# Performance work log

Hardware: AMD Instinct MI355X
Metric: run time of the kernel (lower is better)

Reference implementation:

```python
import jax, jax.numpy as jnp
import numpy as np

EPS = 1e-4

@jax.custom_vjp
def bin_active(x):
    # BinActive: sign forward, straight-through (hard-tanh) backward
    return jnp.sign(x)

def _ba_fwd(x):
    return jnp.sign(x), x

def _ba_bwd(x, g):
    return (g * (jnp.abs(x) <= 1.0).astype(g.dtype),)

bin_active.defvjp(_ba_fwd, _ba_bwd)

def norm_bin(x):
    # per-node mean/std (torch .std is unbiased, ddof=1) then binarize
    x = x - jnp.mean(x, axis=1, keepdims=True)
    x = x / (jnp.std(x, axis=1, ddof=1, keepdims=True) + EPS)
    return bin_active(x)

def bin_weight(W):
    # XNOR-style weight binarization: per-output-row scale * sign(W)
    alpha = jnp.mean(jnp.abs(W), axis=1, keepdims=True)
    return alpha * jnp.sign(W)

def bi_sage_conv(x_src, x_tgt, edge_index, W_l, W_r, b):
    # mean-aggregate source messages onto targets, then two binarized linears
    src, dst = edge_index[0], edge_index[1]
    n_tgt = x_tgt.shape[0]
    msg = x_src[src]                                             # [E, F] gather
    agg = jax.ops.segment_sum(msg, dst, num_segments=n_tgt)       # [n_tgt, F]
    cnt = jax.ops.segment_sum(jnp.ones((src.shape[0],), x_src.dtype), dst,
                              num_segments=n_tgt)
    agg = agg / jnp.maximum(cnt, 1.0)[:, None]
    out = agg @ bin_weight(W_l).T + x_tgt @ bin_weight(W_r).T + b
    return out


def setup_inputs() -> dict:
    key = jax.random.key(0)
    ks = jax.random.split(key, 10)
    N0, N1, B = 292864, 11264, 1024
    F_IN, F_HID, F_OUT = 602, 256, 41
    E1, E2 = 281600, 10240
    x = jax.random.normal(ks[0], (N0, F_IN), dtype=jnp.float32)
    # bipartite edges: row0 = source idx in [0, n_src), row1 = target idx in [0, n_tgt)
    ei1 = jnp.stack([jax.random.randint(ks[1], (E1,), 0, N0),
                     jax.random.randint(ks[2], (E1,), 0, N1)]).astype(jnp.int64)
    ei2 = jnp.stack([jax.random.randint(ks[3], (E2,), 0, N1),
                     jax.random.randint(ks[4], (E2,), 0, B)]).astype(jnp.int64)
    s1 = 0.1
    return {
        "x": x,
        "edge_index1": ei1,
        "edge_index2": ei2,
        "n1": N1,
        "n_batch": B,
        "W1_l": s1 * jax.random.normal(ks[5], (F_HID, F_IN), dtype=jnp.float32),
        "W1_r": s1 * jax.random.normal(ks[6], (F_HID, F_IN), dtype=jnp.float32),
        "b1": jnp.zeros((F_HID,), jnp.float32),
        "W2_l": s1 * jax.random.normal(ks[7], (F_OUT, F_HID), dtype=jnp.float32),
        "W2_r": s1 * jax.random.normal(ks[8], (F_OUT, F_HID), dtype=jnp.float32),
        "b2": jnp.zeros((F_OUT,), jnp.float32),
    }


def reference(x, edge_index1, edge_index2, n1, n_batch,
              W1_l, W1_r, b1, W2_l, W2_r, b2):
    # layer 1
    x_t = x[:n1]
    h = bi_sage_conv(norm_bin(x), norm_bin(x_t), edge_index1, W1_l, W1_r, b1)
    h = jax.nn.relu(h)  # dropout p=0.0 -> identity
    # layer 2
    h_t = h[:n_batch]
    out = bi_sage_conv(norm_bin(h), norm_bin(h_t), edge_index2, W2_l, W2_r, b2)
    return jax.nn.log_softmax(out, axis=-1)
```

## Files before the change

kernel.cpp:

```cpp
#include <hip/hip_runtime.h>
#include <hip/hip_bf16.h>
#include <cstdint>
#include <cstddef>

#define CDIV(a,b) (((a)+(b)-1)/(b))

using bf16x8 = __attribute__((ext_vector_type(8))) short;
using f32x4  = __attribute__((ext_vector_type(4))) float;

struct __align__(8) F4 { float x, y, z, w; };
struct __align__(8) F2 { float x, y; };

__device__ __forceinline__ unsigned short sgn_bf16(float s){
  return (s > 0.f) ? 0x3F80u : ((s < 0.f) ? 0xBF80u : 0u);
}

__device__ __forceinline__ int colX(int k){
  int w = k >> 5, b = k & 31;
  if (w < 16){
    int g = w >> 3, wr = w & 7;
    int j = wr >> 1, half = wr & 1;
    return 256*g + 4*(32*half + b) + j;
  }
  int j = w - 16;
  int c = 512 + 4*b + j;
  return (c < 602) ? c : -1;
}
__device__ __forceinline__ int colH(int k){
  int w = k >> 5, b = k & 31;
  int j = w >> 1, half = w & 1;
  return 4*(32*half + b) + j;
}

__global__ void prep_all(const float* __restrict__ W1l, const float* __restrict__ W1r,
                         const float* __restrict__ W2l, const float* __restrict__ W2r,
                         float* __restrict__ aL, float* __restrict__ aR,
                         float* __restrict__ a2L, float* __restrict__ a2R,
                         int* __restrict__ degB, int ndeg,
                         unsigned short* __restrict__ bsgn,
                         unsigned char* __restrict__ mask, int n0, int n1){
  int r = blockIdx.x;
  if (r < 594){
    const float* wr; float* dst; int K;
    if (r < 256){ wr = W1l + (size_t)r*602; dst = aL + r; K = 602; }
    else if (r < 512){ int q = r-256; wr = W1r + (size_t)q*602; dst = aR + q; K = 602; }
    else if (r < 553){ int q = r-512; wr = W2l + (size_t)q*256; dst = a2L + q; K = 256; }
    else { int q = r-553; wr = W2r + (size_t)q*256; dst = a2R + q; K = 256; }
    float s = 0.f;
    for (int k = threadIdx.x; k < K; k += blockDim.x) s += fabsf(wr[k]);
    #pragma unroll
    for (int off = 32; off; off >>= 1) s += __shfl_xor(s, off);
    __shared__ float red[4];
    int wid = threadIdx.x >> 6, lane = threadIdx.x & 63;
    if (lane == 0) red[wid] = s;
    __syncthreads();
    if (threadIdx.x == 0) *dst = (red[0]+red[1]+red[2]+red[3]) / (float)K;
  } else if (r < 642){
    int i = (r - 594)*256 + threadIdx.x;
    if (i < ndeg) degB[i] = 0;
  } else if (r < 1922){
    int idx = (r - 642)*256 + threadIdx.x;
    if (idx < 256*1280){
      int o = idx / 1280, k = idx - o*1280;
      float v = 0.f;
      if (k < 640){ int c = colX(k);       if (c >= 0) v = W1l[(size_t)o*602 + c]; }
      else        { int c = colX(k - 640); if (c >= 0) v = W1r[(size_t)o*602 + c]; }
      bsgn[idx] = sgn_bf16(v);
    }
  } else {
    int i = (r - 1922)*256 + threadIdx.x;
    if (i < n0) mask[i] = (i < n1) ? 1 : 0;
  }
}

__global__ void mark_count(const int* __restrict__ s1, const int* __restrict__ d1, int E1,
                           unsigned char* __restrict__ mask, int* __restrict__ deg1,
                           const int* __restrict__ d2, int E2, int* __restrict__ deg2){
  int e = blockIdx.x*blockDim.x + threadIdx.x;
  if (e < E1){
    mask[s1[e]] = 1;
    atomicAdd(&deg1[d1[e]], 1);
  } else if (e < E1 + E2){
    atomicAdd(&deg2[d2[e - E1]], 1);
  }
}

__global__ void pack_scan_bcat(const float* __restrict__ X, uint32_t* __restrict__ P, int nrows,
                               const unsigned char* __restrict__ mask, int packBlocks,
                               const int* __restrict__ deg1, int* __restrict__ rs1, int* __restrict__ cur1, int n1c,
                               const int* __restrict__ deg2, int* __restrict__ rs2, int* __restrict__ cur2, int n2c,
                               const float* __restrict__ W2l, const float* __restrict__ W2r,
                               const float* __restrict__ a2L, const float* __restrict__ a2R,
                               float* __restrict__ Bcat2){
  __shared__ int partial[256];
  const int bid = blockIdx.x;
  if (bid >= packBlocks){
    int role = bid - packBlocks;
    if (role < 2){
      const int* deg = role ? deg2 : deg1;
      int* rs  = role ? rs2  : rs1;
      int* cur = role ? cur2 : cur1;
      int n    = role ? n2c  : n1c;
      int tid = threadIdx.x;
      int per = CDIV(n, 256);
      int begin = tid*per; if (begin > n) begin = n;
      int end = begin + per; if (end > n) end = n;
      int s = 0;
      for (int i = begin; i < end; ++i) s += deg[i];
      partial[tid] = s;
      __syncthreads();
      for (int off = 1; off < 256; off <<= 1){
        int add = (tid >= off) ? partial[tid-off] : 0;
        __syncthreads();
        partial[tid] += add;
        __syncthreads();
      }
      int prefix = (tid == 0) ? 0 : partial[tid-1];
      for (int i = begin; i < end; ++i){ rs[i] = prefix; cur[i] = prefix; prefix += deg[i]; }
      if (tid == 255) rs[n] = prefix;
    } else {
      int idx = (role - 2)*256 + threadIdx.x;
      if (idx < 512*41){
        int o = idx % 41, k = idx / 41;
        int c = (k < 256) ? colH(k) : colH(k - 256);
        float w = (k < 256) ? W2l[(size_t)o*256 + c] : W2r[(size_t)o*256 + c];
        float a = (k < 256) ? a2L[o] : a2R[o];
        float sg = (w > 0.f) ? 1.f : ((w < 0.f) ? -1.f : 0.f);
        Bcat2[idx] = a * sg;
      }
    }
    return;
  }
  const int row = bid*4 + (threadIdx.x >> 6);
  const int lane = threadIdx.x & 63;
  if (row >= nrows) return;
  if (!mask[row]) return;
  const float* xr = X + (size_t)row * 602;
  F4 v0 = *(const F4*)&xr[4*lane];
  F4 v1 = *(const F4*)&xr[256 + 4*lane];
  F4 v2 = {0.f,0.f,0.f,0.f};
  if (lane < 22) v2 = *(const F4*)&xr[512 + 4*lane];
  else if (lane == 22){ F2 t = *(const F2*)&xr[600]; v2.x = t.x; v2.y = t.y; }
  float s = v0.x+v0.y+v0.z+v0.w + v1.x+v1.y+v1.z+v1.w + v2.x+v2.y+v2.z+v2.w;
  #pragma unroll
  for (int off = 32; off; off >>= 1) s += __shfl_xor(s, off);
  const float mean = s / 602.f;
  uint32_t wpos[20], wneg[20];
  {
    float d0 = v0.x - mean, d1v = v0.y - mean, d2v = v0.z - mean, d3 = v0.w - mean;
    unsigned long long b0 = __ballot(d0 > 0.f), b1 = __ballot(d1v > 0.f),
                       b2 = __ballot(d2v > 0.f), b3 = __ballot(d3 > 0.f);
    wpos[0]=(uint32_t)b0; wpos[1]=(uint32_t)(b0>>32); wpos[2]=(uint32_t)b1; wpos[3]=(uint32_t)(b1>>32);
    wpos[4]=(uint32_t)b2; wpos[5]=(uint32_t)(b2>>32); wpos[6]=(uint32_t)b3; wpos[7]=(uint32_t)(b3>>32);
    b0 = __ballot(d0 < 0.f); b1 = __ballot(d1v < 0.f); b2 = __ballot(d2v < 0.f); b3 = __ballot(d3 < 0.f);
    wneg[0]=(uint32_t)b0; wneg[1]=(uint32_t)(b0>>32); wneg[2]=(uint32_t)b1; wneg[3]=(uint32_t)(b1>>32);
    wneg[4]=(uint32_t)b2; wneg[5]=(uint32_t)(b2>>32); wneg[6]=(uint32_t)b3; wneg[7]=(uint32_t)(b3>>32);
  }
  {
    float d0 = v1.x - mean, d1v = v1.y - mean, d2v = v1.z - mean, d3 = v1.w - mean;
    unsigned long long b0 = __ballot(d0 > 0.f), b1 = __ballot(d1v > 0.f),
                       b2 = __ballot(d2v > 0.f), b3 = __ballot(d3 > 0.f);
    wpos[8]=(uint32_t)b0; wpos[9]=(uint32_t)(b0>>32); wpos[10]=(uint32_t)b1; wpos[11]=(uint32_t)(b1>>32);
    wpos[12]=(uint32_t)b2; wpos[13]=(uint32_t)(b2>>32); wpos[14]=(uint32_t)b3; wpos[15]=(uint32_t)(b3>>32);
    b0 = __ballot(d0 < 0.f); b1 = __ballot(d1v < 0.f); b2 = __ballot(d2v < 0.f); b3 = __ballot(d3 < 0.f);
    wneg[8]=(uint32_t)b0; wneg[9]=(uint32_t)(b0>>32); wneg[10]=(uint32_t)b1; wneg[11]=(uint32_t)(b1>>32);
    wneg[12]=(uint32_t)b2; wneg[13]=(uint32_t)(b2>>32); wneg[14]=(uint32_t)b3; wneg[15]=(uint32_t)(b3>>32);
  }
  {
    int base = 4*lane;
    float d0 = v2.x - mean, d1v = v2.y - mean, d2v = v2.z - mean, d3 = v2.w - mean;
    wpos[16] = (uint32_t)__ballot((base+0 < 90) && (d0 > 0.f));
    wpos[17] = (uint32_t)__ballot((base+1 < 90) && (d1v > 0.f));
    wpos[18] = (uint32_t)__ballot((base+2 < 90) && (d2v > 0.f));
    wpos[19] = (uint32_t)__ballot((base+3 < 90) && (d3 > 0.f));
    wneg[16] = (uint32_t)__ballot((base+0 < 90) && (d0 < 0.f));
    wneg[17] = (uint32_t)__ballot((base+1 < 90) && (d1v < 0.f));
    wneg[18] = (uint32_t)__ballot((base+2 < 90) && (d2v < 0.f));
    wneg[19] = (uint32_t)__ballot((base+3 < 90) && (d3 < 0.f));
  }
  if (lane == 0){
    uint32_t* pr = P + (size_t)row * 40;
    #pragma unroll
    for (int q = 0; q < 5; ++q){
      uint4 a; a.x = wpos[4*q]; a.y = wpos[4*q+1]; a.z = wpos[4*q+2]; a.w = wpos[4*q+3];
      *(uint4*)&pr[4*q] = a;
      uint4 b; b.x = wneg[4*q]; b.y = wneg[4*q+1]; b.z = wneg[4*q+2]; b.w = wneg[4*q+3];
      *(uint4*)&pr[20 + 4*q] = b;
    }
  }
}

__global__ void fill_both(const int* __restrict__ s1, const int* __restrict__ d1, int E1,
                          int* __restrict__ cur1, int* __restrict__ esrc1,
                          const int* __restrict__ s2, const int* __restrict__ d2, int E2,
                          int* __restrict__ cur2, int* __restrict__ esrc2){
  int e = blockIdx.x*blockDim.x + threadIdx.x;
  if (e < E1){
    int p = atomicAdd(&cur1[d1[e]], 1);
    esrc1[p] = s1[e];
  } else if (e < E1 + E2){
    int q = e - E1;
    int p = atomicAdd(&cur2[d2[q]], 1);
    esrc2[p] = s2[q];
  }
}

__global__ void aggregate_v3(const uint32_t* __restrict__ packed,
                             const int* __restrict__ rs, const int* __restrict__ esrc,
                             unsigned short* __restrict__ S, float* __restrict__ invdeg){
  const int t = blockIdx.x;
  const int lane = threadIdx.x;
  const int slot = lane / 20;
  const int w = lane - slot*20;
  const int s0 = rs[t], s1 = rs[t+1];
  const bool active = slot < 3;
  uint32_t p[8] = {0,0,0,0,0,0,0,0};
  uint32_t n[8] = {0,0,0,0,0,0,0,0};
  for (int base = s0; base < s1; base += 3){
    int e = base + slot;
    uint32_t wp = 0, wn = 0;
    if (active && e < s1){
      const uint32_t* pr = packed + (size_t)esrc[e] * 40;
      wp = pr[w];
      wn = pr[20 + w];
    }
    #pragma unroll
    for (int b = 0; b < 8; ++b){
      p[b] += (wp >> b) & 0x01010101u;
      n[b] += (wn >> b) & 0x01010101u;
    }
  }
  #pragma unroll
  for (int b = 0; b < 8; ++b){
    p[b] += __shfl(p[b], lane + 20) + __shfl(p[b], lane + 40);
    n[b] += __shfl(n[b], lane + 20) + __shfl(n[b], lane + 40);
  }
  if (lane == 0){
    int deg = s1 - s0;
    invdeg[t] = 1.f / (float)(deg > 0 ? deg : 1);
  }
  if (lane < 20){
    unsigned short* sr = S + (size_t)t * 640;
    #pragma unroll
    for (int b = 0; b < 8; ++b){
      #pragma unroll
      for (int k = 0; k < 4; ++k){
        int col = 32*lane + b + 8*k;
        int cnt = (int)((p[b] >> (8*k)) & 0xFF) - (int)((n[b] >> (8*k)) & 0xFF);
        float f = (float)cnt;
        sr[col] = (unsigned short)(__float_as_uint(f) >> 16);
      }
    }
  }
}

__global__ __launch_bounds__(256) void gemm1_fused(
    const unsigned short* __restrict__ Sx, const uint32_t* __restrict__ packedX,
    const unsigned short* __restrict__ bsgn, const float* __restrict__ invdeg,
    const float* __restrict__ aL, const float* __restrict__ aR,
    const float* __restrict__ bias, uint32_t* __restrict__ packedH){
  __shared__ __align__(16) char smem[33792];
  unsigned short (*As)[40] = (unsigned short (*)[40])smem;
  unsigned short (*Bs)[40] = (unsigned short (*)[40])(smem + 32*40*2);
  float (*Hs)[264] = (float (*)[264])smem;

  const int tid = threadIdx.x;
  const int lane = tid & 63, wid = tid >> 6;
  const int m0 = blockIdx.x * 32;
  const int frow = lane & 15, fk = (lane >> 4) * 8;
  const int sRow = tid >> 3, sK = (tid & 7) * 4;

  f32x4 acc1[2][4], acc2[2][4];
  #pragma unroll
  for (int i = 0; i < 2; ++i)
    #pragma unroll
    for (int j = 0; j < 4; ++j){ f32x4 z = {0.f,0.f,0.f,0.f}; acc1[i][j] = z; acc2[i][j] = z; }

  const unsigned short* SxRow = Sx + (size_t)(m0 + sRow) * 640;
  const uint32_t* pxRow = packedX + (size_t)(m0 + sRow) * 40;
  const unsigned short* bsgnCol = bsgn + (size_t)tid * 1280;

  for (int kc = 0; kc < 640; kc += 32){
    *(uint2*)&As[sRow][sK] = *(const uint2*)&SxRow[kc + sK];
    *(bf16x8*)&Bs[tid][0]  = *(const bf16x8*)&bsgnCol[kc];
    *(bf16x8*)&Bs[tid][8]  = *(const bf16x8*)&bsgnCol[kc + 8];
    *(bf16x8*)&Bs[tid][16] = *(const bf16x8*)&bsgnCol[kc + 16];
    *(bf16x8*)&Bs[tid][24] = *(const bf16x8*)&bsgnCol[kc + 24];
    __syncthreads();
    bf16x8 a0 = *(bf16x8*)&As[frow][fk];
    bf16x8 a1 = *(bf16x8*)&As[16 + frow][fk];
    #pragma unroll
    for (int nf = 0; nf < 4; ++nf){
      bf16x8 b = *(bf16x8*)&Bs[wid*64 + nf*16 + frow][fk];
      acc1[0][nf] = __builtin_amdgcn_mfma_f32_16x16x32_bf16(a0, b, acc1[0][nf], 0, 0, 0);
      acc1[1][nf] = __builtin_amdgcn_mfma_f32_16x16x32_bf16(a1, b, acc1[1][nf], 0, 0, 0);
    }
    __syncthreads();
  }
  for (int kc = 0; kc < 640; kc += 32){
    int w = kc >> 5;
    {
      uint32_t wp = pxRow[w];
      uint32_t wq = pxRow[20 + w];
      union { unsigned short u[4]; uint2 v; } tmp;
      #pragma unroll
      for (int j = 0; j < 4; ++j){
        int b_ = sK + j;
        tmp.u[j] = ((wp >> b_) & 1) ? 0x3F80u : (((wq >> b_) & 1) ? 0xBF80u : 0u);
      }
      *(uint2*)&As[sRow][sK] = tmp.v;
    }
    *(bf16x8*)&Bs[tid][0]  = *(const bf16x8*)&bsgnCol[640 + kc];
    *(bf16x8*)&Bs[tid][8]  = *(const bf16x8*)&bsgnCol[640 + kc + 8];
    *(bf16x8*)&Bs[tid][16] = *(const bf16x8*)&bsgnCol[640 + kc + 16];
    *(bf16x8*)&Bs[tid][24] = *(const bf16x8*)&bsgnCol[640 + kc + 24];
    __syncthreads();
    bf16x8 a0 = *(bf16x8*)&As[frow][fk];
    bf16x8 a1 = *(bf16x8*)&As[16 + frow][fk];
    #pragma unroll
    for (int nf = 0; nf < 4; ++nf){
      bf16x8 b = *(bf16x8*)&Bs[wid*64 + nf*16 + frow][fk];
      acc2[0][nf] = __builtin_amdgcn_mfma_f32_16x16x32_bf16(a0, b, acc2[0][nf], 0, 0, 0);
      acc2[1][nf] = __builtin_amdgcn_mfma_f32_16x16x32_bf16(a1, b, acc2[1][nf], 0, 0, 0);
    }
    __syncthreads();
  }

  #pragma unroll
  for (int nf = 0; nf < 4; ++nf){
    int gc = wid*64 + nf*16 + frow;
    float al = aL[gc], ar = aR[gc], bb = bias[gc];
    #pragma unroll
    for (int mf = 0; mf < 2; ++mf){
      #pragma unroll
      for (int reg = 0; reg < 4; ++reg){
        int lr = mf*16 + (lane >> 4)*4 + reg;
        float v = invdeg[m0 + lr]*al*acc1[mf][nf][reg] + ar*acc2[mf][nf][reg] + bb;
        Hs[lr][gc] = fmaxf(v, 0.f);
      }
    }
  }
  __syncthreads();

  for (int r = 0; r < 8; ++r){
    int row = wid*8 + r;
    float4 v = *(const float4*)&Hs[row][4*lane];
    float s = v.x + v.y + v.z + v.w;
    #pragma unroll
    for (int off = 32; off; off >>= 1) s += __shfl_xor(s, off);
    float mean = s * (1.f/256.f);
    float d0 = v.x - mean, d1v = v.y - mean, d2v = v.z - mean, d3 = v.w - mean;
    unsigned long long b0 = __ballot(d0 > 0.f), b1 = __ballot(d1v > 0.f),
                       b2 = __ballot(d2v > 0.f), b3 = __ballot(d3 > 0.f);
    uint32_t wpos[8], wneg[8];
    wpos[0]=(uint32_t)b0; wpos[1]=(uint32_t)(b0>>32); wpos[2]=(uint32_t)b1; wpos[3]=(uint32_t)(b1>>32);
    wpos[4]=(uint32_t)b2; wpos[5]=(uint32_t)(b2>>32); wpos[6]=(uint32_t)b3; wpos[7]=(uint32_t)(b3>>32);
    b0 = __ballot(d0 < 0.f); b1 = __ballot(d1v < 0.f); b2 = __ballot(d2v < 0.f); b3 = __ballot(d3 < 0.f);
    wneg[0]=(uint32_t)b0; wneg[1]=(uint32_t)(b0>>32); wneg[2]=(uint32_t)b1; wneg[3]=(uint32_t)(b1>>32);
    wneg[4]=(uint32_t)b2; wneg[5]=(uint32_t)(b2>>32); wneg[6]=(uint32_t)b3; wneg[7]=(uint32_t)(b3>>32);
    if (lane == 0){
      uint32_t* pr = packedH + (size_t)(m0 + row) * 16;
      *(uint4*)&pr[0]  = make_uint4(wpos[0], wpos[1], wpos[2], wpos[3]);
      *(uint4*)&pr[4]  = make_uint4(wpos[4], wpos[5], wpos[6], wpos[7]);
      *(uint4*)&pr[8]  = make_uint4(wneg[0], wneg[1], wneg[2], wneg[3]);
      *(uint4*)&pr[12] = make_uint4(wneg[4], wneg[5], wneg[6], wneg[7]);
    }
  }
}

__global__ void agg_gemm2(const uint32_t* __restrict__ packedH,
                          const int* __restrict__ rs, const int* __restrict__ esrc,
                          const float* __restrict__ Bcat2, const float* __restrict__ bias,
                          float* __restrict__ out){
  const int t = blockIdx.x;
  const int lane = threadIdx.x;
  const int slot = lane >> 3, w = lane & 7;
  __shared__ float av[512];
  const int s0 = rs[t], s1 = rs[t+1];
  uint32_t p[8] = {0,0,0,0,0,0,0,0};
  uint32_t n[8] = {0,0,0,0,0,0,0,0};
  for (int base = s0; base < s1; base += 8){
    int e = base + slot;
    uint32_t wp = 0, wn = 0;
    if (e < s1){
      const uint32_t* pr = packedH + (size_t)esrc[e] * 16;
      wp = pr[w];
      wn = pr[8 + w];
    }
    #pragma unroll
    for (int b = 0; b < 8; ++b){
      p[b] += (wp >> b) & 0x01010101u;
      n[b] += (wn >> b) & 0x01010101u;
    }
  }
  #pragma unroll
  for (int b = 0; b < 8; ++b){
    p[b] += __shfl_xor(p[b], 8);  p[b] += __shfl_xor(p[b], 16);  p[b] += __shfl_xor(p[b], 32);
    n[b] += __shfl_xor(n[b], 8);  n[b] += __shfl_xor(n[b], 16);  n[b] += __shfl_xor(n[b], 32);
  }
  int deg = s1 - s0;
  float inv = 1.f / (float)(deg > 0 ? deg : 1);
  if (lane < 8){
    #pragma unroll
    for (int b = 0; b < 8; ++b){
      #pragma unroll
      for (int k = 0; k < 4; ++k){
        int col = 32*lane + b + 8*k;
        int cnt = (int)((p[b] >> (8*k)) & 0xFF) - (int)((n[b] >> (8*k)) & 0xFF);
        av[col] = (float)cnt * inv;
      }
    }
  }
  const uint32_t* pr = packedH + (size_t)t * 16;
  for (int k = lane; k < 256; k += 64){
    int wq = k >> 5, b = k & 31;
    av[256 + k] = (float)((pr[wq] >> b) & 1) - (float)((pr[8 + wq] >> b) & 1);
  }
  __syncthreads();
  bool activeO = lane < 41;
  float acc = activeO ? bias[lane] : 0.f;
  for (int k = 0; k < 512; ++k){
    float bw = activeO ? Bcat2[k*41 + lane] : 0.f;
    acc += av[k] * bw;
  }
  float v = activeO ? acc : -INFINITY;
  float m = v;
  #pragma unroll
  for (int off = 32; off; off >>= 1) m = fmaxf(m, __shfl_xor(m, off));
  float e = activeO ? expf(v - m) : 0.f;
  float ssum = e;
  #pragma unroll
  for (int off = 32; off; off >>= 1) ssum += __shfl_xor(ssum, off);
  if (activeO) out[(size_t)t*41 + lane] = v - m - logf(ssum);
}

extern "C" void kernel_launch(void* const* d_in, const int* in_sizes, int n_in,
                              void* d_out, int out_size, void* d_ws, size_t ws_size,
                              hipStream_t stream){
  (void)n_in; (void)out_size; (void)ws_size;
  const float* x   = (const float*)d_in[0];
  const int*   ei1 = (const int*)d_in[1];
  const int*   ei2 = (const int*)d_in[2];
  const float* W1l = (const float*)d_in[5];
  const float* W1r = (const float*)d_in[6];
  const float* b1  = (const float*)d_in[7];
  const float* W2l = (const float*)d_in[8];
  const float* W2r = (const float*)d_in[9];
  const float* b2  = (const float*)d_in[10];
  float* out = (float*)d_out;

  const int FIN = 602, N1 = 11264, NB = 1024;
  const int N0 = in_sizes[0] / FIN;
  const int E1 = in_sizes[1] / 2;
  const int E2 = in_sizes[2] / 2;

  char* wsb = (char*)d_ws;
  size_t off = 0;
  auto carve = [&](size_t bytes)->void*{
    void* p = wsb + off;
    off = (off + bytes + 255) & ~(size_t)255;
    return p;
  };
  uint32_t* packedX = (uint32_t*)carve((size_t)N0*40*4);
  uint32_t* packedH = (uint32_t*)carve((size_t)N1*16*4);
  unsigned short* Sx = (unsigned short*)carve((size_t)N1*640*2);
  float* invdeg1 = (float*)carve((size_t)N1*4);
  unsigned short* bsgn = (unsigned short*)carve((size_t)256*1280*2);
  float* Bcat2 = (float*)carve((size_t)512*41*4);
  float* aL  = (float*)carve(256*4);
  float* aR  = (float*)carve(256*4);
  float* a2L = (float*)carve(64*4);
  float* a2R = (float*)carve(64*4);
  unsigned char* mask = (unsigned char*)carve((size_t)N0);
  int* degB  = (int*)carve((size_t)(N1+NB)*4);
  int* deg1  = degB;
  int* deg2  = degB + N1;
  int* rs1   = (int*)carve((size_t)(N1+1)*4);
  int* cur1  = (int*)carve((size_t)N1*4);
  int* esrc1 = (int*)carve((size_t)E1*4);
  int* rs2   = (int*)carve((size_t)(NB+1)*4);
  int* cur2  = (int*)carve((size_t)NB*4);
  int* esrc2 = (int*)carve((size_t)E2*4);

  const int maskBlocks = CDIV(N0, 256);
  const int cntBlocks  = CDIV(E1 + E2, 256);
  const int packBlocks = CDIV(N0, 4);
  const int bcatBlocks = CDIV(512*41, 256);

  prep_all<<<1922 + maskBlocks, 256, 0, stream>>>(
      W1l, W1r, W2l, W2r, aL, aR, a2L, a2R, degB, N1 + NB, bsgn, mask, N0, N1);
  mark_count<<<cntBlocks, 256, 0, stream>>>(ei1, ei1 + E1, E1, mask, deg1,
                                            ei2 + E2, E2, deg2);
  pack_scan_bcat<<<packBlocks + 2 + bcatBlocks, 256, 0, stream>>>(
      x, packedX, N0, mask, packBlocks,
      deg1, rs1, cur1, N1, deg2, rs2, cur2, NB,
      W2l, W2r, a2L, a2R, Bcat2);
  fill_both<<<cntBlocks, 256, 0, stream>>>(ei1, ei1 + E1, E1, cur1, esrc1,
                                           ei2, ei2 + E2, E2, cur2, esrc2);
  aggregate_v3<<<N1, 64, 0, stream>>>(packedX, rs1, esrc1, Sx, invdeg1);
  gemm1_fused<<<N1/32, 256, 0, stream>>>(Sx, packedX, bsgn, invdeg1, aL, aR, b1, packedH);
  agg_gemm2<<<NB, 64, 0, stream>>>(packedH, rs2, esrc2, Bcat2, b2, out);
}
```

Before: 277.3 us.

## Fuse all pipeline stages into one cooperative persistent kernel with grid syncs

Result: slower. 1.079 ms (+289.3%).

```diff
diff --git a/kernel.cpp b/kernel.cpp
--- a/kernel.cpp
+++ b/kernel.cpp
@@ -1,8 +1,10 @@
 #include <hip/hip_runtime.h>
-#include <hip/hip_bf16.h>
+#include <hip/hip_cooperative_groups.h>
 #include <cstdint>
 #include <cstddef>
 
+namespace cg = cooperative_groups;
+
 #define CDIV(a,b) (((a)+(b)-1)/(b))
 
 using bf16x8 = __attribute__((ext_vector_type(8))) short;
@@ -10,6 +12,9 @@
 
 struct __align__(8) F4 { float x, y, z, w; };
 struct __align__(8) F2 { float x, y; };
+
+#define N1C 11264
+#define NBC 1024
 
 __device__ __forceinline__ unsigned short sgn_bf16(float s){
   return (s > 0.f) ? 0x3F80u : ((s < 0.f) ? 0xBF80u : 0u);
@@ -32,424 +37,427 @@
   return 4*(32*half + b) + j;
 }
 
-__global__ void prep_all(const float* __restrict__ W1l, const float* __restrict__ W1r,
-                         const float* __restrict__ W2l, const float* __restrict__ W2r,
-                         float* __restrict__ aL, float* __restrict__ aR,
-                         float* __restrict__ a2L, float* __restrict__ a2R,
-                         int* __restrict__ degB, int ndeg,
-                         unsigned short* __restrict__ bsgn,
-                         unsigned char* __restrict__ mask, int n0, int n1){
-  int r = blockIdx.x;
-  if (r < 594){
-    const float* wr; float* dst; int K;
-    if (r < 256){ wr = W1l + (size_t)r*602; dst = aL + r; K = 602; }
-    else if (r < 512){ int q = r-256; wr = W1r + (size_t)q*602; dst = aR + q; K = 602; }
-    else if (r < 553){ int q = r-512; wr = W2l + (size_t)q*256; dst = a2L + q; K = 256; }
-    else { int q = r-553; wr = W2r + (size_t)q*256; dst = a2R + q; K = 256; }
-    float s = 0.f;
-    for (int k = threadIdx.x; k < K; k += blockDim.x) s += fabsf(wr[k]);
-    #pragma unroll
-    for (int off = 32; off; off >>= 1) s += __shfl_xor(s, off);
-    __shared__ float red[4];
-    int wid = threadIdx.x >> 6, lane = threadIdx.x & 63;
-    if (lane == 0) red[wid] = s;
-    __syncthreads();
-    if (threadIdx.x == 0) *dst = (red[0]+red[1]+red[2]+red[3]) / (float)K;
-  } else if (r < 642){
-    int i = (r - 594)*256 + threadIdx.x;
-    if (i < ndeg) degB[i] = 0;
-  } else if (r < 1922){
-    int idx = (r - 642)*256 + threadIdx.x;
-    if (idx < 256*1280){
-      int o = idx / 1280, k = idx - o*1280;
-      float v = 0.f;
-      if (k < 640){ int c = colX(k);       if (c >= 0) v = W1l[(size_t)o*602 + c]; }
-      else        { int c = colX(k - 640); if (c >= 0) v = W1r[(size_t)o*602 + c]; }
-      bsgn[idx] = sgn_bf16(v);
-    }
-  } else {
-    int i = (r - 1922)*256 + threadIdx.x;
-    if (i < n0) mask[i] = (i < n1) ? 1 : 0;
-  }
-}
-
-__global__ void mark_count(const int* __restrict__ s1, const int* __restrict__ d1, int E1,
-                           unsigned char* __restrict__ mask, int* __restrict__ deg1,
-                           const int* __restrict__ d2, int E2, int* __restrict__ deg2){
-  int e = blockIdx.x*blockDim.x + threadIdx.x;
-  if (e < E1){
-    mask[s1[e]] = 1;
-    atomicAdd(&deg1[d1[e]], 1);
-  } else if (e < E1 + E2){
-    atomicAdd(&deg2[d2[e - E1]], 1);
-  }
-}
-
-__global__ void pack_scan_bcat(const float* __restrict__ X, uint32_t* __restrict__ P, int nrows,
-                               const unsigned char* __restrict__ mask, int packBlocks,
-                               const int* __restrict__ deg1, int* __restrict__ rs1, int* __restrict__ cur1, int n1c,
-                               const int* __restrict__ deg2, int* __restrict__ rs2, int* __restrict__ cur2, int n2c,
-                               const float* __restrict__ W2l, const float* __restrict__ W2r,
-                               const float* __restrict__ a2L, const float* __restrict__ a2R,
-                               float* __restrict__ Bcat2){
-  __shared__ int partial[256];
-  const int bid = blockIdx.x;
-  if (bid >= packBlocks){
-    int role = bid - packBlocks;
-    if (role < 2){
-      const int* deg = role ? deg2 : deg1;
-      int* rs  = role ? rs2  : rs1;
-      int* cur = role ? cur2 : cur1;
-      int n    = role ? n2c  : n1c;
-      int tid = threadIdx.x;
-      int per = CDIV(n, 256);
-      int begin = tid*per; if (begin > n) begin = n;
-      int end = begin + per; if (end > n) end = n;
-      int s = 0;
-      for (int i = begin; i < end; ++i) s += deg[i];
-      partial[tid] = s;
+struct KParams {
+  const float* x; const int* ei1; const int* ei2;
+  const float* W1l; const float* W1r; const float* b1;
+  const float* W2l; const float* W2r; const float* b2;
+  float* out;
+  uint32_t* packedX; uint32_t* packedH;
+  unsigned short* Sx; float* invdeg;
+  unsigned short* bsgn; float* Bcat2;
+  float* aL; float* aR; float* a2L; float* a2R;
+  unsigned char* mask;
+  int* deg1; int* deg2;
+  int* rs1; int* cur1; int* esrc1;
+  int* rs2; int* cur2; int* esrc2;
+  int N0, E1, E2;
+};
+
+__global__ __launch_bounds__(256, 4) void mega(KParams P){
+  cg::grid_group grid = cg::this_grid();
+  __shared__ __align__(16) char smem[33792];
+  const int tid  = threadIdx.x;
+  const int lane = tid & 63, wid = tid >> 6;
+  const int gsz  = (int)gridDim.x;
+
+  {
+    const int maskBlocks = CDIV(P.N0, 256);
+    const int total = 594 + maskBlocks + CDIV(N1C + NBC, 256);
+    for (int vb = blockIdx.x; vb < total; vb += gsz){
+      if (vb < 594){
+        const float* wr; float* dst; int K;
+        if (vb < 256){ wr = P.W1l + (size_t)vb*602; dst = P.aL + vb; K = 602; }
+        else if (vb < 512){ int q = vb-256; wr = P.W1r + (size_t)q*602; dst = P.aR + q; K = 602; }
+        else if (vb < 553){ int q = vb-512; wr = P.W2l + (size_t)q*256; dst = P.a2L + q; K = 256; }
+        else { int q = vb-553; wr = P.W2r + (size_t)q*256; dst = P.a2R + q; K = 256; }
+        float s = 0.f;
+        for (int k = tid; k < K; k += 256) s += fabsf(wr[k]);
+        #pragma unroll
+        for (int off = 32; off; off >>= 1) s += __shfl_xor(s, off);
+        float* red = (float*)smem;
+        if (lane == 0) red[wid] = s;
+        __syncthreads();
+        if (tid == 0) *dst = (red[0]+red[1]+red[2]+red[3]) / (float)K;
+        __syncthreads();
+      } else if (vb < 594 + maskBlocks){
+        int i = (vb-594)*256 + tid;
+        if (i < P.N0) P.mask[i] = (i < N1C) ? 1 : 0;
+      } else {
+        int i = (vb - 594 - maskBlocks)*256 + tid;
+        if (i < N1C + NBC) P.deg1[i] = 0;
+      }
+    }
+  }
+  __threadfence(); grid.sync();
+
+  {
+    const int cntBlocks = CDIV(P.E1 + P.E2, 256);
+    const int total = cntBlocks + 1280 + CDIV(512*41, 256);
+    for (int vb = blockIdx.x; vb < total; vb += gsz){
+      if (vb < cntBlocks){
+        int e = vb*256 + tid;
+        if (e < P.E1){
+          P.mask[P.ei1[e]] = 1;
+          atomicAdd(&P.deg1[P.ei1[P.E1 + e]], 1);
+        } else if (e < P.E1 + P.E2){
+          int q = e - P.E1;
+          atomicAdd(&P.deg2[P.ei2[P.E2 + q]], 1);
+        }
+      } else if (vb < cntBlocks + 1280){
+        int idx = (vb - cntBlocks)*256 + tid;
+        int o = idx / 1280, k = idx - o*1280;
+        float v = 0.f;
+        if (k < 640){ int c = colX(k);       if (c >= 0) v = P.W1l[(size_t)o*602 + c]; }
+        else        { int c = colX(k - 640); if (c >= 0) v = P.W1r[(size_t)o*602 + c]; }
+        P.bsgn[idx] = sgn_bf16(v);
+      } else {
+        int idx = (vb - cntBlocks - 1280)*256 + tid;
+        if (idx < 512*41){
+          int o = idx % 41, k = idx / 41;
+          int c = (k < 256) ? colH(k) : colH(k - 256);
+          float w = (k < 256) ? P.W2l[(size_t)o*256 + c] : P.W2r[(size_t)o*256 + c];
+          float a = (k < 256) ? P.a2L[o] : P.a2R[o];
+          float sg = (w > 0.f) ? 1.f : ((w < 0.f) ? -1.f : 0.f);
+          P.Bcat2[idx] = a * sg;
+        }
+      }
+    }
+  }
+  __threadfence(); grid.sync();
+
+  {
+    const int packBlocks = CDIV(P.N0, 4);
+    const int total = packBlocks + 2;
+    for (int vb = blockIdx.x; vb < total; vb += gsz){
+      if (vb < packBlocks){
+        int row = vb*4 + wid;
+        if (row < P.N0 && P.mask[row]){
+          const float* xr = P.x + (size_t)row * 602;
+          F4 v0 = *(const F4*)&xr[4*lane];
+          F4 v1 = *(const F4*)&xr[256 + 4*lane];
+          F4 v2 = {0.f,0.f,0.f,0.f};
+          if (lane < 22) v2 = *(const F4*)&xr[512 + 4*lane];
+          else if (lane == 22){ F2 t = *(const F2*)&xr[600]; v2.x = t.x; v2.y = t.y; }
+          float s = v0.x+v0.y+v0.z+v0.w + v1.x+v1.y+v1.z+v1.w + v2.x+v2.y+v2.z+v2.w;
+          #pragma unroll
+          for (int off = 32; off; off >>= 1) s += __shfl_xor(s, off);
+          const float mean = s / 602.f;
+          uint32_t wpos[20], wneg[20];
+          {
+            float d0 = v0.x - mean, d1v = v0.y - mean, d2v = v0.z - mean, d3 = v0.w - mean;
+            unsigned long long b0 = __ballot(d0 > 0.f), b1 = __ballot(d1v > 0.f),
+                               b2 = __ballot(d2v > 0.f), b3 = __ballot(d3 > 0.f);
+            wpos[0]=(uint32_t)b0; wpos[1]=(uint32_t)(b0>>32); wpos[2]=(uint32_t)b1; wpos[3]=(uint32_t)(b1>>32);
+            wpos[4]=(uint32_t)b2; wpos[5]=(uint32_t)(b2>>32); wpos[6]=(uint32_t)b3; wpos[7]=(uint32_t)(b3>>32);
+            b0 = __ballot(d0 < 0.f); b1 = __ballot(d1v < 0.f); b2 = __ballot(d2v < 0.f); b3 = __ballot(d3 < 0.f);
+            wneg[0]=(uint32_t)b0; wneg[1]=(uint32_t)(b0>>32); wneg[2]=(uint32_t)b1; wneg[3]=(uint32_t)(b1>>32);
+            wneg[4]=(uint32_t)b2; wneg[5]=(uint32_t)(b2>>32); wneg[6]=(uint32_t)b3; wneg[7]=(uint32_t)(b3>>32);
+          }
+          {
+            float d0 = v1.x - mean, d1v = v1.y - mean, d2v = v1.z - mean, d3 = v1.w - mean;
+            unsigned long long b0 = __ballot(d0 > 0.f), b1 = __ballot(d1v > 0.f),
+                               b2 = __ballot(d2v > 0.f), b3 = __ballot(d3 > 0.f);
+            wpos[8]=(uint32_t)b0; wpos[9]=(uint32_t)(b0>>32); wpos[10]=(uint32_t)b1; wpos[11]=(uint32_t)(b1>>32);
+            wpos[12]=(uint32_t)b2; wpos[13]=(uint32_t)(b2>>32); wpos[14]=(uint32_t)b3; wpos[15]=(uint32_t)(b3>>32);
+            b0 = __ballot(d0 < 0.f); b1 = __ballot(d1v < 0.f); b2 = __ballot(d2v < 0.f); b3 = __ballot(d3 < 0.f);
+            wneg[8]=(uint32_t)b0; wneg[9]=(uint32_t)(b0>>32); wneg[10]=(uint32_t)b1; wneg[11]=(uint32_t)(b1>>32);
+            wneg[12]=(uint32_t)b2; wneg[13]=(uint32_t)(b2>>32); wneg[14]=(uint32_t)b3; wneg[15]=(uint32_t)(b3>>32);
+          }
+          {
+            int base = 4*lane;
+            float d0 = v2.x - mean, d1v = v2.y - mean, d2v = v2.z - mean, d3 = v2.w - mean;
+            wpos[16] = (uint32_t)__ballot((base+0 < 90) && (d0 > 0.f));
+            wpos[17] = (uint32_t)__ballot((base+1 < 90) && (d1v > 0.f));
+            wpos[18] = (uint32_t)__ballot((base+2 < 90) && (d2v > 0.f));
+            wpos[19] = (uint32_t)__ballot((base+3 < 90) && (d3 > 0.f));
+            wneg[16] = (uint32_t)__ballot((base+0 < 90) && (d0 < 0.f));
+            wneg[17] = (uint32_t)__ballot((base+1 < 90) && (d1v < 0.f));
+            wneg[18] = (uint32_t)__ballot((base+2 < 90) && (d2v < 0.f));
+            wneg[19] = (uint32_t)__ballot((base+3 < 90) && (d3 < 0.f));
+          }
+          if (lane == 0){
+            uint32_t* pr = P.packedX + (size_t)row * 40;
+            #pragma unroll
+            for (int q = 0; q < 5; ++q){
+              uint4 a; a.x = wpos[4*q]; a.y = wpos[4*q+1]; a.z = wpos[4*q+2]; a.w = wpos[4*q+3];
+              *(uint4*)&pr[4*q] = a;
+              uint4 b; b.x = wneg[4*q]; b.y = wneg[4*q+1]; b.z = wneg[4*q+2]; b.w = wneg[4*q+3];
+              *(uint4*)&pr[20 + 4*q] = b;
+            }
+          }
+        }
+      } else {
+        int role = vb - packBlocks;
+        const int* deg = role ? P.deg2 : P.deg1;
+        int* rs  = role ? P.rs2  : P.rs1;
+        int* cur = role ? P.cur2 : P.cur1;
+        int n    = role ? NBC    : N1C;
+        int* partial = (int*)smem;
+        int per = CDIV(n, 256);
+        int begin = tid*per; if (begin > n) begin = n;
+        int end = begin + per; if (end > n) end = n;
+        int s = 0;
+        for (int i = begin; i < end; ++i) s += deg[i];
+        partial[tid] = s;
+        __syncthreads();
+        for (int off = 1; off < 256; off <<= 1){
+          int add = (tid >= off) ? partial[tid-off] : 0;
+          __syncthreads();
+          partial[tid] += add;
+          __syncthreads();
+        }
+        int prefix = (tid == 0) ? 0 : partial[tid-1];
+        for (int i = begin; i < end; ++i){ rs[i] = prefix; cur[i] = prefix; prefix += deg[i]; }
+        if (tid == 255) rs[n] = prefix;
+        __syncthreads();
+      }
+    }
+  }
+  __threadfence(); grid.sync();
+
+  {
+    const int cntBlocks = CDIV(P.E1 + P.E2, 256);
+    for (int vb = blockIdx.x; vb < cntBlocks; vb += gsz){
+      int e = vb*256 + tid;
+      if (e < P.E1){
+        int pos = atomicAdd(&P.cur1[P.ei1[P.E1 + e]], 1);
+        P.esrc1[pos] = P.ei1[e];
+      } else if (e < P.E1 + P.E2){
+        int q = e - P.E1;
+        int pos = atomicAdd(&P.cur2[P.ei2[P.E2 + q]], 1);
+        P.esrc2[pos] = P.ei2[q];
+      }
+    }
+  }
+  __threadfence(); grid.sync();
+
+  {
+    for (int vb = blockIdx.x; vb < N1C/4; vb += gsz){
+      int t = vb*4 + wid;
+      const int slot = lane / 20;
+      const int w = lane - slot*20;
+      const int s0 = P.rs1[t], s1 = P.rs1[t+1];
+      const bool act = slot < 3;
+      uint32_t pp[8] = {0,0,0,0,0,0,0,0};
+      uint32_t nn[8] = {0,0,0,0,0,0,0,0};
+      for (int base = s0; base < s1; base += 3){
+        int e = base + slot;
+        uint32_t wp = 0, wn = 0;
+        if (act && e < s1){
+          const uint32_t* pr = P.packedX + (size_t)P.esrc1[e] * 40;
+          wp = pr[w]; wn = pr[20 + w];
+        }
+        #pragma unroll
+        for (int b = 0; b < 8; ++b){
+          pp[b] += (wp >> b) & 0x01010101u;
+          nn[b] += (wn >> b) & 0x01010101u;
+        }
+      }
+      #pragma unroll
+      for (int b = 0; b < 8; ++b){
+        pp[b] += __shfl(pp[b], lane + 20) + __shfl(pp[b], lane + 40);
+        nn[b] += __shfl(nn[b], lane + 20) + __shfl(nn[b], lane + 40);
+      }
+      if (lane == 0){
+        int deg = s1 - s0;
+        P.invdeg[t] = 1.f / (float)(deg > 0 ? deg : 1);
+      }
+      if (lane < 20){
+        unsigned short* sr = P.Sx + (size_t)t * 640;
+        #pragma unroll
+        for (int b = 0; b < 8; ++b){
+          #pragma unroll
+          for (int k = 0; k < 4; ++k){
+            int col = 32*lane + b + 8*k;
+            int cnt = (int)((pp[b] >> (8*k)) & 0xFF) - (int)((nn[b] >> (8*k)) & 0xFF);
+            float f = (float)cnt;
+            sr[col] = (unsigned short)(__float_as_uint(f) >> 16);
+          }
+        }
+      }
+    }
+  }
+  __threadfence(); grid.sync();
+
+  {
+    unsigned short (*As)[40] = (unsigned short (*)[40])smem;
+    unsigned short (*Bs)[40] = (unsigned short (*)[40])(smem + 32*40*2);
+    float (*Hs)[264] = (float (*)[264])smem;
+    const int frow = lane & 15, fk = (lane >> 4) * 8;
+    const int sRow = tid >> 3, sK = (tid & 7) * 4;
+    for (int vb = blockIdx.x; vb < N1C/32; vb += gsz){
+      const int m0 = vb * 32;
+      f32x4 acc1[2][4], acc2[2][4];
+      #pragma unroll
+      for (int i = 0; i < 2; ++i)
+        #pragma unroll
+        for (int j = 0; j < 4; ++j){ f32x4 z = {0.f,0.f,0.f,0.f}; acc1[i][j] = z; acc2[i][j] = z; }
+      const unsigned short* SxRow = P.Sx + (size_t)(m0 + sRow) * 640;
+      const uint32_t* pxRow = P.packedX + (size_t)(m0 + sRow) * 40;
+      const unsigned short* bsgnCol = P.bsgn + (size_t)tid * 1280;
+
+      for (int kc = 0; kc < 640; kc += 32){
+        *(uint2*)&As[sRow][sK] = *(const uint2*)&SxRow[kc + sK];
+        *(bf16x8*)&Bs[tid][0]  = *(const bf16x8*)&bsgnCol[kc];
+        *(bf16x8*)&Bs[tid][8]  = *(const bf16x8*)&bsgnCol[kc + 8];
+        *(bf16x8*)&Bs[tid][16] = *(const bf16x8*)&bsgnCol[kc + 16];
+        *(bf16x8*)&Bs[tid][24] = *(const bf16x8*)&bsgnCol[kc + 24];
+        __syncthreads();
+        bf16x8 a0 = *(bf16x8*)&As[frow][fk];
+        bf16x8 a1 = *(bf16x8*)&As[16 + frow][fk];
+        #pragma unroll
+        for (int nf = 0; nf < 4; ++nf){
+          bf16x8 b = *(bf16x8*)&Bs[wid*64 + nf*16 + frow][fk];
+          acc1[0][nf] = __builtin_amdgcn_mfma_f32_16x16x32_bf16(a0, b, acc1[0][nf], 0, 0, 0);
+          acc1[1][nf] = __builtin_amdgcn_mfma_f32_16x16x32_bf16(a1, b, acc1[1][nf], 0, 0, 0);
+        }
+        __syncthreads();
+      }
+      for (int kc = 0; kc < 640; kc += 32){
+        int w = kc >> 5;
+        {
+          uint32_t wp = pxRow[w];
+          uint32_t wq = pxRow[20 + w];
+          union { unsigned short u[4]; uint2 v; } tmp;
+          #pragma unroll
+          for (int j = 0; j < 4; ++j){
+            int b_ = sK + j;
+            tmp.u[j] = ((wp >> b_) & 1) ? 0x3F80u : (((wq >> b_) & 1) ? 0xBF80u : 0u);
+          }
+          *(uint2*)&As[sRow][sK] = tmp.v;
+        }
+        *(bf16x8*)&Bs[tid][0]  = *(const bf16x8*)&bsgnCol[640 + kc];
+        *(bf16x8*)&Bs[tid][8]  = *(const bf16x8*)&bsgnCol[640 + kc + 8];
+        *(bf16x8*)&Bs[tid][16] = *(const bf16x8*)&bsgnCol[640 + kc + 16];
+        *(bf16x8*)&Bs[tid][24] = *(const bf16x8*)&bsgnCol[640 + kc + 24];
+        __syncthreads();
+        bf16x8 a0 = *(bf16x8*)&As[frow][fk];
+        bf16x8 a1 = *(bf16x8*)&As[16 + frow][fk];
+        #pragma unroll
+        for (int nf = 0; nf < 4; ++nf){
+          bf16x8 b = *(bf16x8*)&Bs[wid*64 + nf*16 + frow][fk];
+          acc2[0][nf] = __builtin_amdgcn_mfma_f32_16x16x32_bf16(a0, b, acc2[0][nf], 0, 0, 0);
+          acc2[1][nf] = __builtin_amdgcn_mfma_f32_16x16x32_bf16(a1, b, acc2[1][nf], 0, 0, 0);
+        }
+        __syncthreads();
+      }
+
+      #pragma unroll
+      for (int nf = 0; nf < 4; ++nf){
+        int gc = wid*64 + nf*16 + frow;
+        float al = P.aL[gc], ar = P.aR[gc], bb = P.b1[gc];
+        #pragma unroll
+        for (int mf = 0; mf < 2; ++mf){
+          #pragma unroll
+          for (int reg = 0; reg < 4; ++reg){
+            int lr = mf*16 + (lane >> 4)*4 + reg;
+            float v = P.invdeg[m0 + lr]*al*acc1[mf][nf][reg] + ar*acc2[mf][nf][reg] + bb;
+            Hs[lr][gc] = fmaxf(v, 0.f);
+          }
+        }
+      }
       __syncthreads();
-      for (int off = 1; off < 256; off <<= 1){
-        int add = (tid >= off) ? partial[tid-off] : 0;
-        __syncthreads();
-        partial[tid] += add;
-        __syncthreads();
-      }
-      int prefix = (tid == 0) ? 0 : partial[tid-1];
-      for (int i = begin; i < end; ++i){ rs[i] = prefix; cur[i] = prefix; prefix += deg[i]; }
-      if (tid == 255) rs[n] = prefix;
-    } else {
-      int idx = (role - 2)*256 + threadIdx.x;
-      if (idx < 512*41){
-        int o = idx % 41, k = idx / 41;
-        int c = (k < 256) ? colH(k) : colH(k - 256);
-        float w = (k < 256) ? W2l[(size_t)o*256 + c] : W2r[(size_t)o*256 + c];
-        float a = (k < 256) ? a2L[o] : a2R[o];
-        float sg = (w > 0.f) ? 1.f : ((w < 0.f) ? -1.f : 0.f);
-        Bcat2[idx] = a * sg;
-      }
-    }
-    return;
-  }
-  const int row = bid*4 + (threadIdx.x >> 6);
-  const int lane = threadIdx.x & 63;
-  if (row >= nrows) return;
-  if (!mask[row]) return;
-  const float* xr = X + (size_t)row * 602;
-  F4 v0 = *(const F4*)&xr[4*lane];
-  F4 v1 = *(const F4*)&xr[256 + 4*lane];
-  F4 v2 = {0.f,0.f,0.f,0.f};
-  if (lane < 22) v2 = *(const F4*)&xr[512 + 4*lane];
-  else if (lane == 22){ F2 t = *(const F2*)&xr[600]; v2.x = t.x; v2.y = t.y; }
-  float s = v0.x+v0.y+v0.z+v0.w + v1.x+v1.y+v1.z+v1.w + v2.x+v2.y+v2.z+v2.w;
-  #pragma unroll
-  for (int off = 32; off; off >>= 1) s += __shfl_xor(s, off);
-  const float mean = s / 602.f;
-  uint32_t wpos[20], wneg[20];
-  {
-    float d0 = v0.x - mean, d1v = v0.y - mean, d2v = v0.z - mean, d3 = v0.w - mean;
-    unsigned long long b0 = __ballot(d0 > 0.f), b1 = __ballot(d1v > 0.f),
-                       b2 = __ballot(d2v > 0.f), b3 = __ballot(d3 > 0.f);
-    wpos[0]=(uint32_t)b0; wpos[1]=(uint32_t)(b0>>32); wpos[2]=(uint32_t)b1; wpos[3]=(uint32_t)(b1>>32);
-    wpos[4]=(uint32_t)b2; wpos[5]=(uint32_t)(b2>>32); wpos[6]=(uint32_t)b3; wpos[7]=(uint32_t)(b3>>32);
-    b0 = __ballot(d0 < 0.f); b1 = __ballot(d1v < 0.f); b2 = __ballot(d2v < 0.f); b3 = __ballot(d3 < 0.f);
-    wneg[0]=(uint32_t)b0; wneg[1]=(uint32_t)(b0>>32); wneg[2]=(uint32_t)b1; wneg[3]=(uint32_t)(b1>>32);
-    wneg[4]=(uint32_t)b2; wneg[5]=(uint32_t)(b2>>32); wneg[6]=(uint32_t)b3; wneg[7]=(uint32_t)(b3>>32);
-  }
-  {
-    float d0 = v1.x - mean, d1v = v1.y - mean, d2v = v1.z - mean, d3 = v1.w - mean;
-    unsigned long long b0 = __ballot(d0 > 0.f), b1 = __ballot(d1v > 0.f),
-                       b2 = __ballot(d2v > 0.f), b3 = __ballot(d3 > 0.f);
-    wpos[8]=(uint32_t)b0; wpos[9]=(uint32_t)(b0>>32); wpos[10]=(uint32_t)b1; wpos[11]=(uint32_t)(b1>>32);
-    wpos[12]=(uint32_t)b2; wpos[13]=(uint32_t)(b2>>32); wpos[14]=(uint32_t)b3; wpos[15]=(uint32_t)(b3>>32);
-    b0 = __ballot(d0 < 0.f); b1 = __ballot(d1v < 0.f); b2 = __ballot(d2v < 0.f); b3 = __ballot(d3 < 0.f);
-    wneg[8]=(uint32_t)b0; wneg[9]=(uint32_t)(b0>>32); wneg[10]=(uint32_t)b1; wneg[11]=(uint32_t)(b1>>32);
-    wneg[12]=(uint32_t)b2; wneg[13]=(uint32_t)(b2>>32); wneg[14]=(uint32_t)b3; wneg[15]=(uint32_t)(b3>>32);
-  }
-  {
-    int base = 4*lane;
-    float d0 = v2.x - mean, d1v = v2.y - mean, d2v = v2.z - mean, d3 = v2.w - mean;
-    wpos[16] = (uint32_t)__ballot((base+0 < 90) && (d0 > 0.f));
-    wpos[17] = (uint32_t)__ballot((base+1 < 90) && (d1v > 0.f));
-    wpos[18] = (uint32_t)__ballot((base+2 < 90) && (d2v > 0.f));
-    wpos[19] = (uint32_t)__ballot((base+3 < 90) && (d3 > 0.f));
-    wneg[16] = (uint32_t)__ballot((base+0 < 90) && (d0 < 0.f));
-    wneg[17] = (uint32_t)__ballot((base+1 < 90) && (d1v < 0.f));
-    wneg[18] = (uint32_t)__ballot((base+2 < 90) && (d2v < 0.f));
-    wneg[19] = (uint32_t)__ballot((base+3 < 90) && (d3 < 0.f));
-  }
-  if (lane == 0){
-    uint32_t* pr = P + (size_t)row * 40;
-    #pragma unroll
-    for (int q = 0; q < 5; ++q){
-      uint4 a; a.x = wpos[4*q]; a.y = wpos[4*q+1]; a.z = wpos[4*q+2]; a.w = wpos[4*q+3];
-      *(uint4*)&pr[4*q] = a;
-      uint4 b; b.x = wneg[4*q]; b.y = wneg[4*q+1]; b.z = wneg[4*q+2]; b.w = wneg[4*q+3];
-      *(uint4*)&pr[20 + 4*q] = b;
-    }
-  }
-}
-
-__global__ void fill_both(const int* __restrict__ s1, const int* __restrict__ d1, int E1,
-                          int* __restrict__ cur1, int* __restrict__ esrc1,
-                          const int* __restrict__ s2, const int* __restrict__ d2, int E2,
-                          int* __restrict__ cur2, int* __restrict__ esrc2){
-  int e = blockIdx.x*blockDim.x + threadIdx.x;
-  if (e < E1){
-    int p = atomicAdd(&cur1[d1[e]], 1);
-    esrc1[p] = s1[e];
-  } else if (e < E1 + E2){
-    int q = e - E1;
-    int p = atomicAdd(&cur2[d2[q]], 1);
-    esrc2[p] = s2[q];
-  }
-}
-
-__global__ void aggregate_v3(const uint32_t* __restrict__ packed,
-                             const int* __restrict__ rs, const int* __restrict__ esrc,
-                             unsigned short* __restrict__ S, float* __restrict__ invdeg){
-  const int t = blockIdx.x;
-  const int lane = threadIdx.x;
-  const int slot = lane / 20;
-  const int w = lane - slot*20;
-  const int s0 = rs[t], s1 = rs[t+1];
-  const bool active = slot < 3;
-  uint32_t p[8] = {0,0,0,0,0,0,0,0};
-  uint32_t n[8] = {0,0,0,0,0,0,0,0};
-  for (int base = s0; base < s1; base += 3){
-    int e = base + slot;
-    uint32_t wp = 0, wn = 0;
-    if (active && e < s1){
-      const uint32_t* pr = packed + (size_t)esrc[e] * 40;
-      wp = pr[w];
-      wn = pr[20 + w];
-    }
-    #pragma unroll
-    for (int b = 0; b < 8; ++b){
-      p[b] += (wp >> b) & 0x01010101u;
-      n[b] += (wn >> b) & 0x01010101u;
-    }
-  }
-  #pragma unroll
-  for (int b = 0; b < 8; ++b){
-    p[b] += __shfl(p[b], lane + 20) + __shfl(p[b], lane + 40);
-    n[b] += __shfl(n[b], lane + 20) + __shfl(n[b], lane + 40);
-  }
-  if (lane == 0){
-    int deg = s1 - s0;
-    invdeg[t] = 1.f / (float)(deg > 0 ? deg : 1);
-  }
-  if (lane < 20){
-    unsigned short* sr = S + (size_t)t * 640;
-    #pragma unroll
-    for (int b = 0; b < 8; ++b){
+
+      for (int r = 0; r < 8; ++r){
+        int row = wid*8 + r;
+        float4 v = *(const float4*)&Hs[row][4*lane];
+        float s = v.x + v.y + v.z + v.w;
+        #pragma unroll
+        for (int off = 32; off; off >>= 1) s += __shfl_xor(s, off);
+        float mean = s * (1.f/256.f);
+        float d0 = v.x - mean, d1v = v.y - mean, d2v = v.z - mean, d3 = v.w - mean;
+        unsigned long long b0 = __ballot(d0 > 0.f), b1 = __ballot(d1v > 0.f),
+                           b2 = __ballot(d2v > 0.f), b3 = __ballot(d3 > 0.f);
+        uint32_t wpos[8], wneg[8];
+        wpos[0]=(uint32_t)b0; wpos[1]=(uint32_t)(b0>>32); wpos[2]=(uint32_t)b1; wpos[3]=(uint32_t)(b1>>32);
+        wpos[4]=(uint32_t)b2; wpos[5]=(uint32_t)(b2>>32); wpos[6]=(uint32_t)b3; wpos[7]=(uint32_t)(b3>>32);
+        b0 = __ballot(d0 < 0.f); b1 = __ballot(d1v < 0.f); b2 = __ballot(d2v < 0.f); b3 = __ballot(d3 < 0.f);
+        wneg[0]=(uint32_t)b0; wneg[1]=(uint32_t)(b0>>32); wneg[2]=(uint32_t)b1; wneg[3]=(uint32_t)(b1>>32);
+        wneg[4]=(uint32_t)b2; wneg[5]=(uint32_t)(b2>>32); wneg[6]=(uint32_t)b3; wneg[7]=(uint32_t)(b3>>32);
+        if (lane == 0){
+          uint32_t* pr = P.packedH + (size_t)(m0 + row) * 16;
+          *(uint4*)&pr[0]  = make_uint4(wpos[0], wpos[1], wpos[2], wpos[3]);
+          *(uint4*)&pr[4]  = make_uint4(wpos[4], wpos[5], wpos[6], wpos[7]);
+          *(uint4*)&pr[8]  = make_uint4(wneg[0], wneg[1], wneg[2], wneg[3]);
+          *(uint4*)&pr[12] = make_uint4(wneg[4], wneg[5], wneg[6], wneg[7]);
+        }
+      }
+      __syncthreads();
+    }
+  }
+  __threadfence(); grid.sync();
+
+  {
+    float (*av)[512] = (float (*)[512])smem;
+    for (int vb = blockIdx.x; vb < NBC/4; vb += gsz){
+      int t = vb*4 + wid;
+      float* avw = av[wid];
+      const int slot = lane >> 3, w = lane & 7;
+      const int s0 = P.rs2[t], s1 = P.rs2[t+1];
+      uint32_t pp[8] = {0,0,0,0,0,0,0,0};
+      uint32_t nn[8] = {0,0,0,0,0,0,0,0};
+      for (int base = s0; base < s1; base += 8){
+        int e = base + slot;
+        uint32_t wp = 0, wn = 0;
+        if (e < s1){
+          const uint32_t* pr = P.packedH + (size_t)P.esrc2[e] * 16;
+          wp = pr[w]; wn = pr[8 + w];
+        }
+        #pragma unroll
+        for (int b = 0; b < 8; ++b){
+          pp[b] += (wp >> b) & 0x01010101u;
+          nn[b] += (wn >> b) & 0x01010101u;
+        }
+      }
       #pragma unroll
-      for (int k = 0; k < 4; ++k){
-        int col = 32*lane + b + 8*k;
-        int cnt = (int)((p[b] >> (8*k)) & 0xFF) - (int)((n[b] >> (8*k)) & 0xFF);
-        float f = (float)cnt;
-        sr[col] = (unsigned short)(__float_as_uint(f) >> 16);
-      }
-    }
-  }
-}
-
-__global__ __launch_bounds__(256) void gemm1_fused(
-    const unsigned short* __restrict__ Sx, const uint32_t* __restrict__ packedX,
-    const unsigned short* __restrict__ bsgn, const float* __restrict__ invdeg,
-    const float* __restrict__ aL, const float* __restrict__ aR,
-    const float* __restrict__ bias, uint32_t* __restrict__ packedH){
-  __shared__ __align__(16) char smem[33792];
-  unsigned short (*As)[40] = (unsigned short (*)[40])smem;
-  unsigned short (*Bs)[40] = (unsigned short (*)[40])(smem + 32*40*2);
-  float (*Hs)[264] = (float (*)[264])smem;
-
-  const int tid = threadIdx.x;
-  const int lane = tid & 63, wid = tid >> 6;
-  const int m0 = blockIdx.x * 32;
-  const int frow = lane & 15, fk = (lane >> 4) * 8;
-  const int sRow = tid >> 3, sK = (tid & 7) * 4;
-
-  f32x4 acc1[2][4], acc2[2][4];
-  #pragma unroll
-  for (int i = 0; i < 2; ++i)
-    #pragma unroll
-    for (int j = 0; j < 4; ++j){ f32x4 z = {0.f,0.f,0.f,0.f}; acc1[i][j] = z; acc2[i][j] = z; }
-
-  const unsigned short* SxRow = Sx + (size_t)(m0 + sRow) * 640;
-  const uint32_t* pxRow = packedX + (size_t)(m0 + sRow) * 40;
-  const unsigned short* bsgnCol = bsgn + (size_t)tid * 1280;
-
-  for (int kc = 0; kc < 640; kc += 32){
-    *(uint2*)&As[sRow][sK] = *(const uint2*)&SxRow[kc + sK];
-    *(bf16x8*)&Bs[tid][0]  = *(const bf16x8*)&bsgnCol[kc];
-    *(bf16x8*)&Bs[tid][8]  = *(const bf16x8*)&bsgnCol[kc + 8];
-    *(bf16x8*)&Bs[tid][16] = *(const bf16x8*)&bsgnCol[kc + 16];
-    *(bf16x8*)&Bs[tid][24] = *(const bf16x8*)&bsgnCol[kc + 24];
-    __syncthreads();
-    bf16x8 a0 = *(bf16x8*)&As[frow][fk];
-    bf16x8 a1 = *(bf16x8*)&As[16 + frow][fk];
-    #pragma unroll
-    for (int nf = 0; nf < 4; ++nf){
-      bf16x8 b = *(bf16x8*)&Bs[wid*64 + nf*16 + frow][fk];
-      acc1[0][nf] = __builtin_amdgcn_mfma_f32_16x16x32_bf16(a0, b, acc1[0][nf], 0, 0, 0);
-      acc1[1][nf] = __builtin_amdgcn_mfma_f32_16x16x32_bf16(a1, b, acc1[1][nf], 0, 0, 0);
-    }
-    __syncthreads();
-  }
-  for (int kc = 0; kc < 640; kc += 32){
-    int w = kc >> 5;
-    {
-      uint32_t wp = pxRow[w];
-      uint32_t wq = pxRow[20 + w];
-      union { unsigned short u[4]; uint2 v; } tmp;
+      for (int b = 0; b < 8; ++b){
+        pp[b] += __shfl_xor(pp[b], 8);  pp[b] += __shfl_xor(pp[b], 16);  pp[b] += __shfl_xor(pp[b], 32);
+        nn[b] += __shfl_xor(nn[b], 8);  nn[b] += __shfl_xor(nn[b], 16);  nn[b] += __shfl_xor(nn[b], 32);
+      }
+      int deg = s1 - s0;
+      float inv = 1.f / (float)(deg > 0 ? deg : 1);
+      if (lane < 8){
+        #pragma unroll
+        for (int b = 0; b < 8; ++b){
+          #pragma unroll
+          for (int k = 0; k < 4; ++k){
+            int col = 32*lane + b + 8*k;
+            int cnt = (int)((pp[b] >> (8*k)) & 0xFF) - (int)((nn[b] >> (8*k)) & 0xFF);
+            avw[col] = (float)cnt * inv;
+          }
+        }
+      }
+      const uint32_t* pr = P.packedH + (size_t)t * 16;
+      for (int k = lane; k < 256; k += 64){
+        int wq = k >> 5, b = k & 31;
+        avw[256 + k] = (float)((pr[wq] >> b) & 1) - (float)((pr[8 + wq] >> b) & 1);
+      }
+      __syncthreads();
+      bool activeO = lane < 41;
+      float acc = activeO ? P.b2[lane] : 0.f;
+      for (int k = 0; k < 512; ++k){
+        float bw = activeO ? P.Bcat2[k*41 + lane] : 0.f;
+        acc += avw[k] * bw;
+      }
+      float v = activeO ? acc : -INFINITY;
+      float m = v;
       #pragma unroll
-      for (int j = 0; j < 4; ++j){
-        int b_ = sK + j;
-        tmp.u[j] = ((wp >> b_) & 1) ? 0x3F80u : (((wq >> b_) & 1) ? 0xBF80u : 0u);
-      }
-      *(uint2*)&As[sRow][sK] = tmp.v;
-    }
-    *(bf16x8*)&Bs[tid][0]  = *(const bf16x8*)&bsgnCol[640 + kc];
-    *(bf16x8*)&Bs[tid][8]  = *(const bf16x8*)&bsgnCol[640 + kc + 8];
-    *(bf16x8*)&Bs[tid][16] = *(const bf16x8*)&bsgnCol[640 + kc + 16];
-    *(bf16x8*)&Bs[tid][24] = *(const bf16x8*)&bsgnCol[640 + kc + 24];
-    __syncthreads();
-    bf16x8 a0 = *(bf16x8*)&As[frow][fk];
-    bf16x8 a1 = *(bf16x8*)&As[16 + frow][fk];
-    #pragma unroll
-    for (int nf = 0; nf < 4; ++nf){
-      bf16x8 b = *(bf16x8*)&Bs[wid*64 + nf*16 + frow][fk];
-      acc2[0][nf] = __builtin_amdgcn_mfma_f32_16x16x32_bf16(a0, b, acc2[0][nf], 0, 0, 0);
-      acc2[1][nf] = __builtin_amdgcn_mfma_f32_16x16x32_bf16(a1, b, acc2[1][nf], 0, 0, 0);
-    }
-    __syncthreads();
-  }
-
-  #pragma unroll
-  for (int nf = 0; nf < 4; ++nf){
-    int gc = wid*64 + nf*16 + frow;
-    float al = aL[gc], ar = aR[gc], bb = bias[gc];
-    #pragma unroll
-    for (int mf = 0; mf < 2; ++mf){
+      for (int off = 32; off; off >>= 1) m = fmaxf(m, __shfl_xor(m, off));
+      float e = activeO ? expf(v - m) : 0.f;
+      float ssum = e;
       #pragma unroll
-      for (int reg = 0; reg < 4; ++reg){
-        int lr = mf*16 + (lane >> 4)*4 + reg;
-        float v = invdeg[m0 + lr]*al*acc1[mf][nf][reg] + ar*acc2[mf][nf][reg] + bb;
-        Hs[lr][gc] = fmaxf(v, 0.f);
-      }
-    }
-  }
-  __syncthreads();
-
-  for (int r = 0; r < 8; ++r){
-    int row = wid*8 + r;
-    float4 v = *(const float4*)&Hs[row][4*lane];
-    float s = v.x + v.y + v.z + v.w;
-    #pragma unroll
-    for (int off = 32; off; off >>= 1) s += __shfl_xor(s, off);
-    float mean = s * (1.f/256.f);
-    float d0 = v.x - mean, d1v = v.y - mean, d2v = v.z - mean, d3 = v.w - mean;
-    unsigned long long b0 = __ballot(d0 > 0.f), b1 = __ballot(d1v > 0.f),
-                       b2 = __ballot(d2v > 0.f), b3 = __ballot(d3 > 0.f);
-    uint32_t wpos[8], wneg[8];
-    wpos[0]=(uint32_t)b0; wpos[1]=(uint32_t)(b0>>32); wpos[2]=(uint32_t)b1; wpos[3]=(uint32_t)(b1>>32);
-    wpos[4]=(uint32_t)b2; wpos[5]=(uint32_t)(b2>>32); wpos[6]=(uint32_t)b3; wpos[7]=(uint32_t)(b3>>32);
-    b0 = __ballot(d0 < 0.f); b1 = __ballot(d1v < 0.f); b2 = __ballot(d2v < 0.f); b3 = __ballot(d3 < 0.f);
-    wneg[0]=(uint32_t)b0; wneg[1]=(uint32_t)(b0>>32); wneg[2]=(uint32_t)b1; wneg[3]=(uint32_t)(b1>>32);
-    wneg[4]=(uint32_t)b2; wneg[5]=(uint32_t)(b2>>32); wneg[6]=(uint32_t)b3; wneg[7]=(uint32_t)(b3>>32);
-    if (lane == 0){
-      uint32_t* pr = packedH + (size_t)(m0 + row) * 16;
-      *(uint4*)&pr[0]  = make_uint4(wpos[0], wpos[1], wpos[2], wpos[3]);
-      *(uint4*)&pr[4]  = make_uint4(wpos[4], wpos[5], wpos[6], wpos[7]);
-      *(uint4*)&pr[8]  = make_uint4(wneg[0], wneg[1], wneg[2], wneg[3]);
-      *(uint4*)&pr[12] = make_uint4(wneg[4], wneg[5], wneg[6], wneg[7]);
-    }
-  }
-}
-
-__global__ void agg_gemm2(const uint32_t* __restrict__ packedH,
-                          const int* __restrict__ rs, const int* __restrict__ esrc,
-                          const float* __restrict__ Bcat2, const float* __restrict__ bias,
-                          float* __restrict__ out){
-  const int t = blockIdx.x;
-  const int lane = threadIdx.x;
-  const int slot = lane >> 3, w = lane & 7;
-  __shared__ float av[512];
-  const int s0 = rs[t], s1 = rs[t+1];
-  uint32_t p[8] = {0,0,0,0,0,0,0,0};
-  uint32_t n[8] = {0,0,0,0,0,0,0,0};
-  for (int base = s0; base < s1; base += 8){
-    int e = base + slot;
-    uint32_t wp = 0, wn = 0;
-    if (e < s1){
-      const uint32_t* pr = packedH + (size_t)esrc[e] * 16;
-      wp = pr[w];
-      wn = pr[8 + w];
-    }
-    #pragma unroll
-    for (int b = 0; b < 8; ++b){
-      p[b] += (wp >> b) & 0x01010101u;
-      n[b] += (wn >> b) & 0x01010101u;
-    }
-  }
-  #pragma unroll
-  for (int b = 0; b < 8; ++b){
-    p[b] += __shfl_xor(p[b], 8);  p[b] += __shfl_xor(p[b], 16);  p[b] += __shfl_xor(p[b], 32);
-    n[b] += __shfl_xor(n[b], 8);  n[b] += __shfl_xor(n[b], 16);  n[b] += __shfl_xor(n[b], 32);
-  }
-  int deg = s1 - s0;
-  float inv = 1.f / (float)(deg > 0 ? deg : 1);
-  if (lane < 8){
-    #pragma unroll
-    for (int b = 0; b < 8; ++b){
-      #pragma unroll
-      for (int k = 0; k < 4; ++k){
-        int col = 32*lane + b + 8*k;
-        int cnt = (int)((p[b] >> (8*k)) & 0xFF) - (int)((n[b] >> (8*k)) & 0xFF);
-        av[col] = (float)cnt * inv;
-      }
-    }
-  }
-  const uint32_t* pr = packedH + (size_t)t * 16;
-  for (int k = lane; k < 256; k += 64){
-    int wq = k >> 5, b = k & 31;
-    av[256 + k] = (float)((pr[wq] >> b) & 1) - (float)((pr[8 + wq] >> b) & 1);
-  }
-  __syncthreads();
-  bool activeO = lane < 41;
-  float acc = activeO ? bias[lane] : 0.f;
-  for (int k = 0; k < 512; ++k){
-    float bw = activeO ? Bcat2[k*41 + lane] : 0.f;
-    acc += av[k] * bw;
-  }
-  float v = activeO ? acc : -INFINITY;
-  float m = v;
-  #pragma unroll
-  for (int off = 32; off; off >>= 1) m = fmaxf(m, __shfl_xor(m, off));
-  float e = activeO ? expf(v - m) : 0.f;
-  float ssum = e;
-  #pragma unroll
-  for (int off = 32; off; off >>= 1) ssum += __shfl_xor(ssum, off);
-  if (activeO) out[(size_t)t*41 + lane] = v - m - logf(ssum);
+      for (int off = 32; off; off >>= 1) ssum += __shfl_xor(ssum, off);
+      if (activeO) P.out[(size_t)t*41 + lane] = v - m - logf(ssum);
+      __syncthreads();
+    }
+  }
 }
 
 extern "C" void kernel_launch(void* const* d_in, const int* in_sizes, int n_in,
                               void* d_out, int out_size, void* d_ws, size_t ws_size,
                               hipStream_t stream){
   (void)n_in; (void)out_size; (void)ws_size;
-  const float* x   = (const float*)d_in[0];
-  const int*   ei1 = (const int*)d_in[1];
-  const int*   ei2 = (const int*)d_in[2];
-  const float* W1l = (const float*)d_in[5];
-  const float* W1r = (const float*)d_in[6];
-  const float* b1  = (const float*)d_in[7];
-  const float* W2l = (const float*)d_in[8];
-  const float* W2r = (const float*)d_in[9];
-  const float* b2  = (const float*)d_in[10];
-  float* out = (float*)d_out;
-
-  const int FIN = 602, N1 = 11264, NB = 1024;
+  const int FIN = 602;
   const int N0 = in_sizes[0] / FIN;
   const int E1 = in_sizes[1] / 2;
   const int E2 = in_sizes[2] / 2;
@@ -462,9 +470,9 @@
     return p;
   };
   uint32_t* packedX = (uint32_t*)carve((size_t)N0*40*4);
-  uint32_t* packedH = (uint32_t*)carve((size_t)N1*16*4);
-  unsigned short* Sx = (unsigned short*)carve((size_t)N1*640*2);
-  float* invdeg1 = (float*)carve((size_t)N1*4);
+  uint32_t* packedH = (uint32_t*)carve((size_t)N1C*16*4);
+  unsigned short* Sx = (unsigned short*)carve((size_t)N1C*640*2);
+  float* invdeg = (float*)carve((size_t)N1C*4);
   unsigned short* bsgn = (unsigned short*)carve((size_t)256*1280*2);
   float* Bcat2 = (float*)carve((size_t)512*41*4);
   float* aL  = (float*)carve(256*4);
@@ -472,32 +480,41 @@
   float* a2L = (float*)carve(64*4);
   float* a2R = (float*)carve(64*4);
   unsigned char* mask = (unsigned char*)carve((size_t)N0);
-  int* degB  = (int*)carve((size_t)(N1+NB)*4);
-  int* deg1  = degB;
-  int* deg2  = degB + N1;
-  int* rs1   = (int*)carve((size_t)(N1+1)*4);
-  int* cur1  = (int*)carve((size_t)N1*4);
+  int* degB  = (int*)carve((size_t)(N1C+NBC)*4);
+  int* rs1   = (int*)carve((size_t)(N1C+1)*4);
+  int* cur1  = (int*)carve((size_t)N1C*4);
   int* esrc1 = (int*)carve((size_t)E1*4);
-  int* rs2   = (int*)carve((size_t)(NB+1)*4);
-  int* cur2  = (int*)carve((size_t)NB*4);
+  int* rs2   = (int*)carve((size_t)(NBC+1)*4);
+  int* cur2  = (int*)carve((size_t)NBC*4);
   int* esrc2 = (int*)carve((size_t)E2*4);
 
-  const int maskBlocks = CDIV(N0, 256);
-  const int cntBlocks  = CDIV(E1 + E2, 256);
-  const int packBlocks = CDIV(N0, 4);
-  const int bcatBlocks = CDIV(512*41, 256);
-
-  prep_all<<<1922 + maskBlocks, 256, 0, stream>>>(
-      W1l, W1r, W2l, W2r, aL, aR, a2L, a2R, degB, N1 + NB, bsgn, mask, N0, N1);
-  mark_count<<<cntBlocks, 256, 0, stream>>>(ei1, ei1 + E1, E1, mask, deg1,
-                                            ei2 + E2, E2, deg2);
-  pack_scan_bcat<<<packBlocks + 2 + bcatBlocks, 256, 0, stream>>>(
-      x, packedX, N0, mask, packBlocks,
-      deg1, rs1, cur1, N1, deg2, rs2, cur2, NB,
-      W2l, W2r, a2L, a2R, Bcat2);
-  fill_both<<<cntBlocks, 256, 0, stream>>>(ei1, ei1 + E1, E1, cur1, esrc1,
-                                           ei2, ei2 + E2, E2, cur2, esrc2);
-  aggregate_v3<<<N1, 64, 0, stream>>>(packedX, rs1, esrc1, Sx, invdeg1);
-  gemm1_fused<<<N1/32, 256, 0, stream>>>(Sx, packedX, bsgn, invdeg1, aL, aR, b1, packedH);
-  agg_gemm2<<<NB, 64, 0, stream>>>(packedH, rs2, esrc2, Bcat2, b2, out);
+  KParams p;
+  p.x = (const float*)d_in[0];
+  p.ei1 = (const int*)d_in[1];
+  p.ei2 = (const int*)d_in[2];
+  p.W1l = (const float*)d_in[5];
+  p.W1r = (const float*)d_in[6];
+  p.b1  = (const float*)d_in[7];
+  p.W2l = (const float*)d_in[8];
+  p.W2r = (const float*)d_in[9];
+  p.b2  = (const float*)d_in[10];
+  p.out = (float*)d_out;
+  p.packedX = packedX; p.packedH = packedH;
+  p.Sx = Sx; p.invdeg = invdeg;
+  p.bsgn = bsgn; p.Bcat2 = Bcat2;
+  p.aL = aL; p.aR = aR; p.a2L = a2L; p.a2R = a2R;
+  p.mask = mask;
+  p.deg1 = degB; p.deg2 = degB + N1C;
+  p.rs1 = rs1; p.cur1 = cur1; p.esrc1 = esrc1;
+  p.rs2 = rs2; p.cur2 = cur2; p.esrc2 = esrc2;
+  p.N0 = N0; p.E1 = E1; p.E2 = E2;
+
+  int nb = 0;
+  hipOccupancyMaxActiveBlocksPerMultiprocessor(&nb, mega, 256, 0);
+  if (nb < 1) nb = 1;
+  if (nb > 4) nb = 4;
+  int grid = nb * 256;
+
+  void* args[] = { (void*)&p };
+  hipLaunchCooperativeKernel((void*)mega, dim3(grid), dim3(256), args, 0, stream);
 }
```
